# Kernel optimization log

Measured on AMD Instinct MI355X. Metric: run time of the kernel, lower is better.

Reference implementation:

```python
import jax, jax.numpy as jnp
import numpy as np

NBITS = 8
MAXQ = float(2**NBITS - 1)  # 255 for uint8 asymmetric quantization


def asym_quantize(x):
    """Per-tensor asymmetric quantization to the [0, 255] grid.

    x ~ scale * (q - zero), with scale = (max-min)/255, zero = round(-min/scale).
    Returns (q, scale, zero) with q kept in float32 holding integer values.
    """
    xmax = jnp.max(x)
    xmin = jnp.min(x)
    scale = (xmax - xmin) / MAXQ
    zero = jnp.round(-xmin / scale)
    q = jnp.clip(jnp.round(x / scale) + zero, 0.0, MAXQ)
    return q, scale, zero


def setup_inputs() -> dict:
    key = jax.random.key(0)
    kA, kB = jax.random.split(key)
    A = jax.random.normal(kA, (4096, 2048), dtype=jnp.float32)
    B = jax.random.normal(kB, (2048, 4096), dtype=jnp.float32)
    return {"A": A, "B": B}


def reference(A, B):
    # Quantize both operands per-tensor asymmetrically.
    qA, sA, zA = asym_quantize(A)  # [M, K]
    qB, sB, zB = asym_quantize(B)  # [K, N]
    K = A.shape[1]

    # Integer GEMM on the quantized values (exact int accumulation in int32).
    acc = jnp.matmul(qA.astype(jnp.int32), qB.astype(jnp.int32)).astype(jnp.float32)  # [M, N]

    # Fused asymmetric dequant epilogue:
    # A @ B = sA*sB * (qA@qB - zA * colsum(qB) - zB * rowsum(qA) + K*zA*zB)
    rowsum_qA = jnp.sum(qA, axis=1, keepdims=True)   # [M, 1]
    colsum_qB = jnp.sum(qB, axis=0, keepdims=True)   # [1, N]
    out = (sA * sB) * (acc - zA * colsum_qB - zB * rowsum_qA
                       + jnp.float32(K) * zA * zB)
    return out
```

## Files before the change

### kernel.cpp

```cpp
#include <hip/hip_runtime.h>
#include <math.h>


#define M_DIM 4096
#define K_DIM 2048
#define N_DIM 4096

using int4v = __attribute__((ext_vector_type(4))) int;

typedef __attribute__((address_space(1))) const void glb_cv;
typedef __attribute__((address_space(3))) void lds_v;

__device__ __forceinline__ int qbyte(float x, float rs, float z) {
    float q = fminf(fmaxf(rintf(x * rs) + z, 0.0f), 255.0f);
    return (int)q - 128;
}

__device__ __forceinline__ int sum4(int w) {
    return (int)(signed char)(w) + (int)(signed char)(w >> 8) +
           (int)(signed char)(w >> 16) + (int)(signed char)(w >> 24);
}

__global__ void minmax_stage1(const float* __restrict__ A,
                              const float* __restrict__ B,
                              float* __restrict__ partials) {
    int b = blockIdx.x;
    const float* src = (b < 512) ? A : B;
    int lb = (b < 512) ? b : b - 512;
    const float4* v = (const float4*)src + (long)lb * 4096;
    float mn = INFINITY, mx = -INFINITY;
    for (int i = threadIdx.x; i < 4096; i += 256) {
        float4 x = v[i];
        mn = fminf(mn, fminf(fminf(x.x, x.y), fminf(x.z, x.w)));
        mx = fmaxf(mx, fmaxf(fmaxf(x.x, x.y), fmaxf(x.z, x.w)));
    }
    for (int off = 32; off; off >>= 1) {
        mn = fminf(mn, __shfl_down(mn, off));
        mx = fmaxf(mx, __shfl_down(mx, off));
    }
    __shared__ float smn[4], smx[4];
    int w = threadIdx.x >> 6;
    if ((threadIdx.x & 63) == 0) { smn[w] = mn; smx[w] = mx; }
    __syncthreads();
    if (threadIdx.x == 0) {
        mn = fminf(fminf(smn[0], smn[1]), fminf(smn[2], smn[3]));
        mx = fmaxf(fmaxf(smx[0], smx[1]), fmaxf(smx[2], smx[3]));
        partials[2 * b] = mn;
        partials[2 * b + 1] = mx;
    }
}

__global__ void minmax_stage2(const float* __restrict__ partials,
                              float* __restrict__ qp,
                              int* __restrict__ colB) {
    int t = threadIdx.x;
    for (int i = t; i < N_DIM; i += 256) colB[i] = 0;
    float mnA = INFINITY, mxA = -INFINITY, mnB = INFINITY, mxB = -INFINITY;
    for (int i = t; i < 512; i += 256) {
        mnA = fminf(mnA, partials[2 * i]);
        mxA = fmaxf(mxA, partials[2 * i + 1]);
        mnB = fminf(mnB, partials[2 * (i + 512)]);
        mxB = fmaxf(mxB, partials[2 * (i + 512) + 1]);
    }
    for (int off = 32; off; off >>= 1) {
        mnA = fminf(mnA, __shfl_down(mnA, off));
        mxA = fmaxf(mxA, __shfl_down(mxA, off));
        mnB = fminf(mnB, __shfl_down(mnB, off));
        mxB = fmaxf(mxB, __shfl_down(mxB, off));
    }
    __shared__ float s[4][4];
    int w = t >> 6;
    if ((t & 63) == 0) { s[w][0] = mnA; s[w][1] = mxA; s[w][2] = mnB; s[w][3] = mxB; }
    __syncthreads();
    if (t == 0) {
        for (int i = 1; i < 4; i++) {
            mnA = fminf(mnA, s[i][0]); mxA = fmaxf(mxA, s[i][1]);
            mnB = fminf(mnB, s[i][2]); mxB = fmaxf(mxB, s[i][3]);
        }
        float sA = (mxA - mnA) / 255.0f;
        float zA = rintf(-mnA / sA);
        float sB = (mxB - mnB) / 255.0f;
        float zB = rintf(-mnB / sB);
        qp[0] = sA; qp[1] = zA; qp[2] = sB; qp[3] = zB;
        qp[4] = 1.0f / sA; qp[5] = 1.0f / sB;
    }
}

__global__ void quantA_kernel(const float* __restrict__ X,
                              signed char* __restrict__ Q,
                              const float* __restrict__ qp,
                              int* __restrict__ rowA) {
    float rs = qp[4], z = qp[1];
    int t = threadIdx.x;
    long base = (long)blockIdx.x * 4096 + (long)t * 16;
    const float4* v = (const float4*)(X + base);
    union { signed char c[16]; int4 i4; } u;
    int ls = 0;
#pragma unroll
    for (int j = 0; j < 4; j++) {
        float4 x = v[j];
        int q0 = qbyte(x.x, rs, z), q1 = qbyte(x.y, rs, z);
        int q2 = qbyte(x.z, rs, z), q3 = qbyte(x.w, rs, z);
        u.c[j * 4 + 0] = (signed char)q0;
        u.c[j * 4 + 1] = (signed char)q1;
        u.c[j * 4 + 2] = (signed char)q2;
        u.c[j * 4 + 3] = (signed char)q3;
        ls += q0 + q1 + q2 + q3;
    }
    *(int4*)(Q + base) = u.i4;
    for (int off = 32; off; off >>= 1) ls += __shfl_down(ls, off);
    __shared__ int ws[4];
    if ((t & 63) == 0) ws[t >> 6] = ls;
    __syncthreads();
    if (t == 0) rowA[blockIdx.x * 2] = ws[0] + ws[1];
    if (t == 128) rowA[blockIdx.x * 2 + 1] = ws[2] + ws[3];
}

__global__ void quantBT_kernel(const float* __restrict__ B,
                               signed char* __restrict__ BT,
                               const float* __restrict__ qp,
                               int* __restrict__ colB) {
    __shared__ int tile[64][17];
    float rs = qp[5], z = qp[3];
    int k0 = blockIdx.x * 64, n0 = blockIdx.y * 64;
    int t = threadIdx.x;
    int cn = (t & 15) * 4;
    int kg = (t >> 4) * 4;
    int w0 = 0, w1 = 0, w2 = 0, w3 = 0;
#pragma unroll
    for (int r = 0; r < 4; r++) {
        float4 x = *(const float4*)&B[(long)(k0 + kg + r) * N_DIM + n0 + cn];
        w0 |= (qbyte(x.x, rs, z) & 255) << (8 * r);
        w1 |= (qbyte(x.y, rs, z) & 255) << (8 * r);
        w2 |= (qbyte(x.z, rs, z) & 255) << (8 * r);
        w3 |= (qbyte(x.w, rs, z) & 255) << (8 * r);
    }
    int kc = kg >> 2;
    tile[cn + 0][kc] = w0;
    tile[cn + 1][kc] = w1;
    tile[cn + 2][kc] = w2;
    tile[cn + 3][kc] = w3;
    __syncthreads();
    int n2 = t >> 2, kb = (t & 3) * 4;
    int4 v;
    v.x = tile[n2][kb + 0];
    v.y = tile[n2][kb + 1];
    v.z = tile[n2][kb + 2];
    v.w = tile[n2][kb + 3];
    *(int4*)&BT[(long)(n0 + n2) * K_DIM + k0 + (t & 3) * 16] = v;
    int ls = sum4(v.x) + sum4(v.y) + sum4(v.z) + sum4(v.w);
    ls += __shfl_down(ls, 2);
    ls += __shfl_down(ls, 1);
    if ((t & 3) == 0) atomicAdd(&colB[n0 + n2], ls);
}

__global__ __launch_bounds__(256, 3) void gemm_i8(
        const signed char* __restrict__ A8,
        const signed char* __restrict__ B8T,
        const int* __restrict__ rowA,
        const int* __restrict__ colB,
        const float* __restrict__ qp,
        float* __restrict__ out) {
    __shared__ __align__(16) signed char As[128 * 128];
    __shared__ __align__(16) signed char Bs[128 * 128];

    int b = blockIdx.x;
    int xcd = b & 7, i0 = b >> 3;
    int r = xcd + 8 * (i0 >> 6);
    int j = i0 & 63;
    int mt = (r >> 2) * 8 + (j >> 3);
    int nt = (r & 3) * 8 + (j & 7);
    int r0 = mt * 128, c0 = nt * 128;

    int t = threadIdx.x, lane = t & 63, wave = t >> 6;
    int mrow = lane & 15;
    int g = lane >> 4;
    int wm = (wave >> 1) * 64;
    int wn = (wave & 1) * 64;

    int4v acc[4][4];
#pragma unroll
    for (int i = 0; i < 4; i++)
#pragma unroll
        for (int jj = 0; jj < 4; jj++) acc[i][jj] = (int4v){0, 0, 0, 0};

    long aoff[4], boff[4];
#pragma unroll
    for (int jj = 0; jj < 4; jj++) {
        int ch = t + 256 * jj;
        int row = ch >> 3, p = ch & 7;
        int gk = p ^ (row & 7);
        aoff[jj] = (long)(r0 + row) * K_DIM + gk * 16;
        boff[jj] = (long)(c0 + row) * K_DIM + gk * 16;
    }

    int swz = (mrow & 7);

    for (int k0 = 0; k0 < K_DIM; k0 += 128) {
        __syncthreads();
#pragma unroll
        for (int jj = 0; jj < 4; jj++)
            __builtin_amdgcn_global_load_lds((glb_cv*)(A8 + aoff[jj] + k0),
                                             (lds_v*)(As + (t + 256 * jj) * 16), 16, 0, 0);
#pragma unroll
        for (int jj = 0; jj < 4; jj++)
            __builtin_amdgcn_global_load_lds((glb_cv*)(B8T + boff[jj] + k0),
                                             (lds_v*)(Bs + (t + 256 * jj) * 16), 16, 0, 0);
        __syncthreads();

#pragma unroll
        for (int ks = 0; ks < 2; ks++) {
            int c = ks * 4 + g;
            int koff = (c ^ swz) * 16;
            int4v af[4], bf[4];
#pragma unroll
            for (int i = 0; i < 4; i++)
                af[i] = *(const int4v*)&As[(wm + i * 16 + mrow) * 128 + koff];
#pragma unroll
            for (int jj = 0; jj < 4; jj++)
                bf[jj] = *(const int4v*)&Bs[(wn + jj * 16 + mrow) * 128 + koff];
#pragma unroll
            for (int i = 0; i < 4; i++)
#pragma unroll
                for (int jj = 0; jj < 4; jj++)
                    acc[i][jj] = __builtin_amdgcn_mfma_i32_16x16x64_i8(af[i], bf[jj], acc[i][jj], 0, 0, 0);
        }
    }

    float sA = qp[0], zA = qp[1], sB = qp[2], zB = qp[3];
    int cA = 128 - (int)zA, cB = 128 - (int)zB;
    float ss = sA * sB;
    int Kzz = K_DIM * cA * cB;
    int ocol = c0 + wn + mrow;
    int orow = r0 + wm + g * 4;
#pragma unroll
    for (int i = 0; i < 4; i++) {
        int ra[4];
#pragma unroll
        for (int rr = 0; rr < 4; rr++) ra[rr] = cB * rowA[orow + i * 16 + rr] + Kzz;
#pragma unroll
        for (int jj = 0; jj < 4; jj++) {
            int cc = ocol + jj * 16;
            int can = cA * colB[cc];
#pragma unroll
            for (int rr = 0; rr < 4; rr++) {
                int v = acc[i][jj][rr] + ra[rr] + can;
                out[(long)(orow + i * 16 + rr) * N_DIM + cc] = ss * (float)v;
            }
        }
    }
}

extern "C" void kernel_launch(void* const* d_in, const int* in_sizes, int n_in,
                              void* d_out, int out_size, void* d_ws, size_t ws_size,
                              hipStream_t stream) {
    const float* A = (const float*)d_in[0];
    const float* B = (const float*)d_in[1];
    float* out = (float*)d_out;
    char* ws = (char*)d_ws;

    signed char* A8  = (signed char*)ws;
    signed char* B8T = (signed char*)(ws + 8388608);
    int*   rowA      = (int*)(ws + 16777216);
    int*   colB      = (int*)(ws + 16793600);
    float* partials  = (float*)(ws + 16809984);
    float* qp        = (float*)(ws + 16818176);

    minmax_stage1<<<1024, 256, 0, stream>>>(A, B, partials);
    minmax_stage2<<<1, 256, 0, stream>>>(partials, qp, colB);
    quantA_kernel<<<2048, 256, 0, stream>>>(A, A8, qp, rowA);
    quantBT_kernel<<<dim3(32, 64), 256, 0, stream>>>(B, B8T, qp, colB);
    gemm_i8<<<1024, 256, 0, stream>>>(A8, B8T, rowA, colB, qp, out);
}
```

Measured before the change: 162.9 us.

## Fuse quantization kernels and switch GEMM to 32x32x32 int8 MFMA

Merges the min/max finalize, A quantization and B transpose-quantization into one launch in which every block recomputes the global scale and zero point from the partials. The colsum zeroing moves into the first min/max kernel. The GEMM inner loop switches from 16x16x64 to 32x32x32 int8 MFMA tiles, which means fewer LDS fragment loads per MFMA, and the epilogue uses vectorized rowA loads and nontemporal output stores. This removes two kernel launches and their gaps, at the cost of each block redundantly reducing the 1024 partials.

```diff
diff --git a/kernel.cpp b/kernel.cpp
--- a/kernel.cpp
+++ b/kernel.cpp
@@ -7,6 +7,7 @@
 #define N_DIM 4096
 
 using int4v = __attribute__((ext_vector_type(4))) int;
+using int16v = __attribute__((ext_vector_type(16))) int;
 
 typedef __attribute__((address_space(1))) const void glb_cv;
 typedef __attribute__((address_space(3))) void lds_v;
@@ -23,8 +24,10 @@
 
 __global__ void minmax_stage1(const float* __restrict__ A,
                               const float* __restrict__ B,
-                              float* __restrict__ partials) {
+                              float* __restrict__ partials,
+                              int* __restrict__ colB) {
     int b = blockIdx.x;
+    if (b < 16) colB[b * 256 + threadIdx.x] = 0;
     const float* src = (b < 512) ? A : B;
     int lb = (b < 512) ? b : b - 512;
     const float4* v = (const float4*)src + (long)lb * 4096;
@@ -50,11 +53,16 @@
     }
 }
 
-__global__ void minmax_stage2(const float* __restrict__ partials,
-                              float* __restrict__ qp,
-                              int* __restrict__ colB) {
-    int t = threadIdx.x;
-    for (int i = t; i < N_DIM; i += 256) colB[i] = 0;
+__global__ void quant_fused(const float* __restrict__ A,
+                            const float* __restrict__ B,
+                            const float* __restrict__ partials,
+                            signed char* __restrict__ A8,
+                            signed char* __restrict__ B8T,
+                            int* __restrict__ rowA,
+                            int* __restrict__ colB,
+                            float* __restrict__ qp) {
+    int b = blockIdx.x, t = threadIdx.x;
+
     float mnA = INFINITY, mxA = -INFINITY, mnB = INFINITY, mxB = -INFINITY;
     for (int i = t; i < 512; i += 256) {
         mnA = fminf(mnA, partials[2 * i]);
@@ -68,90 +76,79 @@
         mnB = fminf(mnB, __shfl_down(mnB, off));
         mxB = fmaxf(mxB, __shfl_down(mxB, off));
     }
-    __shared__ float s[4][4];
+    __shared__ float sred[4][4];
     int w = t >> 6;
-    if ((t & 63) == 0) { s[w][0] = mnA; s[w][1] = mxA; s[w][2] = mnB; s[w][3] = mxB; }
+    if ((t & 63) == 0) { sred[w][0] = mnA; sred[w][1] = mxA; sred[w][2] = mnB; sred[w][3] = mxB; }
     __syncthreads();
-    if (t == 0) {
-        for (int i = 1; i < 4; i++) {
-            mnA = fminf(mnA, s[i][0]); mxA = fmaxf(mxA, s[i][1]);
-            mnB = fminf(mnB, s[i][2]); mxB = fmaxf(mxB, s[i][3]);
-        }
-        float sA = (mxA - mnA) / 255.0f;
-        float zA = rintf(-mnA / sA);
-        float sB = (mxB - mnB) / 255.0f;
-        float zB = rintf(-mnB / sB);
-        qp[0] = sA; qp[1] = zA; qp[2] = sB; qp[3] = zB;
-        qp[4] = 1.0f / sA; qp[5] = 1.0f / sB;
-    }
-}
-
-__global__ void quantA_kernel(const float* __restrict__ X,
-                              signed char* __restrict__ Q,
-                              const float* __restrict__ qp,
-                              int* __restrict__ rowA) {
-    float rs = qp[4], z = qp[1];
-    int t = threadIdx.x;
-    long base = (long)blockIdx.x * 4096 + (long)t * 16;
-    const float4* v = (const float4*)(X + base);
-    union { signed char c[16]; int4 i4; } u;
-    int ls = 0;
-#pragma unroll
-    for (int j = 0; j < 4; j++) {
-        float4 x = v[j];
-        int q0 = qbyte(x.x, rs, z), q1 = qbyte(x.y, rs, z);
-        int q2 = qbyte(x.z, rs, z), q3 = qbyte(x.w, rs, z);
-        u.c[j * 4 + 0] = (signed char)q0;
-        u.c[j * 4 + 1] = (signed char)q1;
-        u.c[j * 4 + 2] = (signed char)q2;
-        u.c[j * 4 + 3] = (signed char)q3;
-        ls += q0 + q1 + q2 + q3;
-    }
-    *(int4*)(Q + base) = u.i4;
-    for (int off = 32; off; off >>= 1) ls += __shfl_down(ls, off);
-    __shared__ int ws[4];
-    if ((t & 63) == 0) ws[t >> 6] = ls;
+    mnA = fminf(fminf(sred[0][0], sred[1][0]), fminf(sred[2][0], sred[3][0]));
+    mxA = fmaxf(fmaxf(sred[0][1], sred[1][1]), fmaxf(sred[2][1], sred[3][1]));
+    mnB = fminf(fminf(sred[0][2], sred[1][2]), fminf(sred[2][2], sred[3][2]));
+    mxB = fmaxf(fmaxf(sred[0][3], sred[1][3]), fmaxf(sred[2][3], sred[3][3]));
+    float sA = (mxA - mnA) / 255.0f;
+    float zA = rintf(-mnA / sA);
+    float sB = (mxB - mnB) / 255.0f;
+    float zB = rintf(-mnB / sB);
+    if (b == 0 && t == 0) { qp[0] = sA; qp[1] = zA; qp[2] = sB; qp[3] = zB; }
     __syncthreads();
-    if (t == 0) rowA[blockIdx.x * 2] = ws[0] + ws[1];
-    if (t == 128) rowA[blockIdx.x * 2 + 1] = ws[2] + ws[3];
-}
-
-__global__ void quantBT_kernel(const float* __restrict__ B,
-                               signed char* __restrict__ BT,
-                               const float* __restrict__ qp,
-                               int* __restrict__ colB) {
-    __shared__ int tile[64][17];
-    float rs = qp[5], z = qp[3];
-    int k0 = blockIdx.x * 64, n0 = blockIdx.y * 64;
-    int t = threadIdx.x;
-    int cn = (t & 15) * 4;
-    int kg = (t >> 4) * 4;
-    int w0 = 0, w1 = 0, w2 = 0, w3 = 0;
-#pragma unroll
-    for (int r = 0; r < 4; r++) {
-        float4 x = *(const float4*)&B[(long)(k0 + kg + r) * N_DIM + n0 + cn];
-        w0 |= (qbyte(x.x, rs, z) & 255) << (8 * r);
-        w1 |= (qbyte(x.y, rs, z) & 255) << (8 * r);
-        w2 |= (qbyte(x.z, rs, z) & 255) << (8 * r);
-        w3 |= (qbyte(x.w, rs, z) & 255) << (8 * r);
-    }
-    int kc = kg >> 2;
-    tile[cn + 0][kc] = w0;
-    tile[cn + 1][kc] = w1;
-    tile[cn + 2][kc] = w2;
-    tile[cn + 3][kc] = w3;
-    __syncthreads();
-    int n2 = t >> 2, kb = (t & 3) * 4;
-    int4 v;
-    v.x = tile[n2][kb + 0];
-    v.y = tile[n2][kb + 1];
-    v.z = tile[n2][kb + 2];
-    v.w = tile[n2][kb + 3];
-    *(int4*)&BT[(long)(n0 + n2) * K_DIM + k0 + (t & 3) * 16] = v;
-    int ls = sum4(v.x) + sum4(v.y) + sum4(v.z) + sum4(v.w);
-    ls += __shfl_down(ls, 2);
-    ls += __shfl_down(ls, 1);
-    if ((t & 3) == 0) atomicAdd(&colB[n0 + n2], ls);
+
+    if (b < 2048) {
+        float rs = 1.0f / sA, z = zA;
+        long base = (long)b * 4096 + (long)t * 16;
+        const float4* v = (const float4*)(A + base);
+        union { signed char c[16]; int4 i4; } u;
+        int ls = 0;
+#pragma unroll
+        for (int j = 0; j < 4; j++) {
+            float4 x = v[j];
+            int q0 = qbyte(x.x, rs, z), q1 = qbyte(x.y, rs, z);
+            int q2 = qbyte(x.z, rs, z), q3 = qbyte(x.w, rs, z);
+            u.c[j * 4 + 0] = (signed char)q0;
+            u.c[j * 4 + 1] = (signed char)q1;
+            u.c[j * 4 + 2] = (signed char)q2;
+            u.c[j * 4 + 3] = (signed char)q3;
+            ls += q0 + q1 + q2 + q3;
+        }
+        *(int4*)(A8 + base) = u.i4;
+        for (int off = 32; off; off >>= 1) ls += __shfl_down(ls, off);
+        __shared__ int wsum[4];
+        if ((t & 63) == 0) wsum[t >> 6] = ls;
+        __syncthreads();
+        if (t == 0) rowA[b * 2] = wsum[0] + wsum[1];
+        if (t == 128) rowA[b * 2 + 1] = wsum[2] + wsum[3];
+    } else {
+        float rs = 1.0f / sB, z = zB;
+        int bb = b - 2048;
+        int k0 = (bb & 31) * 64, n0 = (bb >> 5) * 64;
+        __shared__ int tile[64][17];
+        int cn = (t & 15) * 4;
+        int kg = (t >> 4) * 4;
+        int w0 = 0, w1 = 0, w2 = 0, w3 = 0;
+#pragma unroll
+        for (int r = 0; r < 4; r++) {
+            float4 x = *(const float4*)&B[(long)(k0 + kg + r) * N_DIM + n0 + cn];
+            w0 |= (qbyte(x.x, rs, z) & 255) << (8 * r);
+            w1 |= (qbyte(x.y, rs, z) & 255) << (8 * r);
+            w2 |= (qbyte(x.z, rs, z) & 255) << (8 * r);
+            w3 |= (qbyte(x.w, rs, z) & 255) << (8 * r);
+        }
+        int kc = kg >> 2;
+        tile[cn + 0][kc] = w0;
+        tile[cn + 1][kc] = w1;
+        tile[cn + 2][kc] = w2;
+        tile[cn + 3][kc] = w3;
+        __syncthreads();
+        int n2 = t >> 2, kb = (t & 3) * 4;
+        int4 v;
+        v.x = tile[n2][kb + 0];
+        v.y = tile[n2][kb + 1];
+        v.z = tile[n2][kb + 2];
+        v.w = tile[n2][kb + 3];
+        *(int4*)&B8T[(long)(n0 + n2) * K_DIM + k0 + (t & 3) * 16] = v;
+        int ls = sum4(v.x) + sum4(v.y) + sum4(v.z) + sum4(v.w);
+        ls += __shfl_down(ls, 2);
+        ls += __shfl_down(ls, 1);
+        if ((t & 3) == 0) atomicAdd(&colB[n0 + n2], ls);
+    }
 }
 
 __global__ __launch_bounds__(256, 3) void gemm_i8(
@@ -166,64 +163,62 @@
 
     int b = blockIdx.x;
     int xcd = b & 7, i0 = b >> 3;
-    int r = xcd + 8 * (i0 >> 6);
-    int j = i0 & 63;
-    int mt = (r >> 2) * 8 + (j >> 3);
-    int nt = (r & 3) * 8 + (j & 7);
+    int reg = xcd + 8 * (i0 >> 6);
+    int jj0 = i0 & 63;
+    int mt = (reg >> 2) * 8 + (jj0 >> 3);
+    int nt = (reg & 3) * 8 + (jj0 & 7);
     int r0 = mt * 128, c0 = nt * 128;
 
     int t = threadIdx.x, lane = t & 63, wave = t >> 6;
-    int mrow = lane & 15;
-    int g = lane >> 4;
+    int l31 = lane & 31;
+    int lh = lane >> 5;
     int wm = (wave >> 1) * 64;
     int wn = (wave & 1) * 64;
 
-    int4v acc[4][4];
-#pragma unroll
-    for (int i = 0; i < 4; i++)
-#pragma unroll
-        for (int jj = 0; jj < 4; jj++) acc[i][jj] = (int4v){0, 0, 0, 0};
+    int16v acc[2][2];
+#pragma unroll
+    for (int i = 0; i < 2; i++)
+#pragma unroll
+        for (int j = 0; j < 2; j++)
+#pragma unroll
+            for (int r = 0; r < 16; r++) acc[i][j][r] = 0;
 
     long aoff[4], boff[4];
 #pragma unroll
-    for (int jj = 0; jj < 4; jj++) {
-        int ch = t + 256 * jj;
+    for (int j = 0; j < 4; j++) {
+        int ch = t + 256 * j;
         int row = ch >> 3, p = ch & 7;
         int gk = p ^ (row & 7);
-        aoff[jj] = (long)(r0 + row) * K_DIM + gk * 16;
-        boff[jj] = (long)(c0 + row) * K_DIM + gk * 16;
-    }
-
-    int swz = (mrow & 7);
+        aoff[j] = (long)(r0 + row) * K_DIM + gk * 16;
+        boff[j] = (long)(c0 + row) * K_DIM + gk * 16;
+    }
+
+    int arow0 = wm + l31, arow1 = wm + 32 + l31;
+    int brow0 = wn + l31, brow1 = wn + 32 + l31;
 
     for (int k0 = 0; k0 < K_DIM; k0 += 128) {
         __syncthreads();
 #pragma unroll
-        for (int jj = 0; jj < 4; jj++)
-            __builtin_amdgcn_global_load_lds((glb_cv*)(A8 + aoff[jj] + k0),
-                                             (lds_v*)(As + (t + 256 * jj) * 16), 16, 0, 0);
-#pragma unroll
-        for (int jj = 0; jj < 4; jj++)
-            __builtin_amdgcn_global_load_lds((glb_cv*)(B8T + boff[jj] + k0),
-                                             (lds_v*)(Bs + (t + 256 * jj) * 16), 16, 0, 0);
-        __syncthreads();
-
-#pragma unroll
-        for (int ks = 0; ks < 2; ks++) {
-            int c = ks * 4 + g;
-            int koff = (c ^ swz) * 16;
-            int4v af[4], bf[4];
-#pragma unroll
-            for (int i = 0; i < 4; i++)
-                af[i] = *(const int4v*)&As[(wm + i * 16 + mrow) * 128 + koff];
-#pragma unroll
-            for (int jj = 0; jj < 4; jj++)
-                bf[jj] = *(const int4v*)&Bs[(wn + jj * 16 + mrow) * 128 + koff];
-#pragma unroll
-            for (int i = 0; i < 4; i++)
-#pragma unroll
-                for (int jj = 0; jj < 4; jj++)
-                    acc[i][jj] = __builtin_amdgcn_mfma_i32_16x16x64_i8(af[i], bf[jj], acc[i][jj], 0, 0, 0);
+        for (int j = 0; j < 4; j++)
+            __builtin_amdgcn_global_load_lds((glb_cv*)(A8 + aoff[j] + k0),
+                                             (lds_v*)(As + (t + 256 * j) * 16), 16, 0, 0);
+#pragma unroll
+        for (int j = 0; j < 4; j++)
+            __builtin_amdgcn_global_load_lds((glb_cv*)(B8T + boff[j] + k0),
+                                             (lds_v*)(Bs + (t + 256 * j) * 16), 16, 0, 0);
+        __syncthreads();
+
+#pragma unroll
+        for (int ks = 0; ks < 4; ks++) {
+            int c = ks * 2 + lh;
+            int4v af0 = *(const int4v*)&As[arow0 * 128 + ((c ^ (arow0 & 7)) * 16)];
+            int4v af1 = *(const int4v*)&As[arow1 * 128 + ((c ^ (arow1 & 7)) * 16)];
+            int4v bf0 = *(const int4v*)&Bs[brow0 * 128 + ((c ^ (brow0 & 7)) * 16)];
+            int4v bf1 = *(const int4v*)&Bs[brow1 * 128 + ((c ^ (brow1 & 7)) * 16)];
+            acc[0][0] = __builtin_amdgcn_mfma_i32_32x32x32_i8(af0, bf0, acc[0][0], 0, 0, 0);
+            acc[0][1] = __builtin_amdgcn_mfma_i32_32x32x32_i8(af0, bf1, acc[0][1], 0, 0, 0);
+            acc[1][0] = __builtin_amdgcn_mfma_i32_32x32x32_i8(af1, bf0, acc[1][0], 0, 0, 0);
+            acc[1][1] = __builtin_amdgcn_mfma_i32_32x32x32_i8(af1, bf1, acc[1][1], 0, 0, 0);
         }
     }
 
@@ -231,21 +226,27 @@
     int cA = 128 - (int)zA, cB = 128 - (int)zB;
     float ss = sA * sB;
     int Kzz = K_DIM * cA * cB;
-    int ocol = c0 + wn + mrow;
-    int orow = r0 + wm + g * 4;
-#pragma unroll
-    for (int i = 0; i < 4; i++) {
-        int ra[4];
-#pragma unroll
-        for (int rr = 0; rr < 4; rr++) ra[rr] = cB * rowA[orow + i * 16 + rr] + Kzz;
-#pragma unroll
-        for (int jj = 0; jj < 4; jj++) {
-            int cc = ocol + jj * 16;
+#pragma unroll
+    for (int fm = 0; fm < 2; fm++) {
+        int rbase = r0 + wm + fm * 32 + 4 * lh;
+        int ra[16];
+#pragma unroll
+        for (int rq = 0; rq < 4; rq++) {
+            int4 rv = *(const int4*)&rowA[rbase + 8 * rq];
+            ra[rq * 4 + 0] = cB * rv.x + Kzz;
+            ra[rq * 4 + 1] = cB * rv.y + Kzz;
+            ra[rq * 4 + 2] = cB * rv.z + Kzz;
+            ra[rq * 4 + 3] = cB * rv.w + Kzz;
+        }
+#pragma unroll
+        for (int fn = 0; fn < 2; fn++) {
+            int cc = c0 + wn + fn * 32 + l31;
             int can = cA * colB[cc];
 #pragma unroll
-            for (int rr = 0; rr < 4; rr++) {
-                int v = acc[i][jj][rr] + ra[rr] + can;
-                out[(long)(orow + i * 16 + rr) * N_DIM + cc] = ss * (float)v;
+            for (int r = 0; r < 16; r++) {
+                int row = rbase + (r & 3) + 8 * (r >> 2);
+                int v = acc[fm][fn][r] + ra[(r >> 2) * 4 + (r & 3)] + can;
+                __builtin_nontemporal_store(ss * (float)v, &out[(long)row * N_DIM + cc]);
             }
         }
     }
@@ -266,9 +267,7 @@
     float* partials  = (float*)(ws + 16809984);
     float* qp        = (float*)(ws + 16818176);
 
-    minmax_stage1<<<1024, 256, 0, stream>>>(A, B, partials);
-    minmax_stage2<<<1, 256, 0, stream>>>(partials, qp, colB);
-    quantA_kernel<<<2048, 256, 0, stream>>>(A, A8, qp, rowA);
-    quantBT_kernel<<<dim3(32, 64), 256, 0, stream>>>(B, B8T, qp, colB);
+    minmax_stage1<<<1024, 256, 0, stream>>>(A, B, partials, colB);
+    quant_fused<<<4096, 256, 0, stream>>>(A, B, partials, A8, B8T, rowA, colB, qp);
     gemm_i8<<<1024, 256, 0, stream>>>(A8, B8T, rowA, colB, qp, out);
 }
```

Result: no change. 164.4 us (+0.9%).
